# Performance work log

Hardware: AMD Instinct MI355X
Metric: run time of the kernel (lower is better)

## Reference

```python
import jax, jax.numpy as jnp
import numpy as np

N = 50000      # nodes
E = 625000     # edges
D_IN = 128     # in_feats
D_OUT = 128    # out_feats


def setup_inputs() -> dict:
    key = jax.random.key(0)
    k1, k2, k3, k4, k5, k6 = jax.random.split(key, 6)
    feat = jax.random.normal(k1, (N, D_IN), dtype=jnp.float32)
    affine = jax.random.uniform(k2, (E,), dtype=jnp.float32)
    src = jax.random.randint(k3, (E,), 0, N, dtype=jnp.int32)
    dst = jnp.sort(jax.random.randint(k4, (E,), 0, N, dtype=jnp.int32))
    # Linear(in_feats*2, out_feats): torch stores weight [out, in]; use [in, out] here
    bound = 1.0 / np.sqrt(2 * D_IN)
    W = jax.random.uniform(k5, (2 * D_IN, D_OUT), minval=-bound, maxval=bound, dtype=jnp.float32)
    b = jax.random.uniform(k6, (D_OUT,), minval=-bound, maxval=bound, dtype=jnp.float32)
    return {"feat": feat, "affine": affine, "src": src, "dst": dst, "W": W, "b": b}


def reference(feat, affine, src, dst, W, b):
    # u_mul_e: per-edge message = srcfeat[src] * edge scalar 'affine'
    msg = feat[src] * affine[:, None]                      # [E, D_IN]
    # fn.sum: scatter-add messages to destination nodes
    agg = jax.ops.segment_sum(msg, dst, num_segments=N)    # [N, D_IN]
    # concat dst features with aggregated neighborhood, then linear
    gcn_feat = jnp.concatenate([feat, agg], axis=-1)       # [N, 2*D_IN]
    return gcn_feat @ W + b                                # [N, D_OUT]
```

## Files before the change

### kernel.cpp

```cpp
#include <hip/hip_runtime.h>

#define N_NODES 50000
#define E_EDGES 625000
#define D 128

typedef __attribute__((ext_vector_type(8)))  short  short8;
typedef __attribute__((ext_vector_type(16))) float  floatx16;

static __device__ inline unsigned short f2bf(float f) {
    union { float f; unsigned u; } v; v.f = f;
    unsigned r = v.u + 0x7FFFu + ((v.u >> 16) & 1u);
    return (unsigned short)(r >> 16);
}
static __device__ inline float bflo(unsigned p) { return __uint_as_float(p << 16); }
static __device__ inline float bfhi(unsigned p) { return __uint_as_float(p & 0xFFFF0000u); }

__global__ __launch_bounds__(256) void prep_kernel(const int* __restrict__ dst,
                                                   const float* __restrict__ W,
                                                   int* __restrict__ rowptr,
                                                   unsigned short* __restrict__ wimg) {
    int t = blockIdx.x * 256 + threadIdx.x;
    if (t <= N_NODES) {
        int lo = 0, hi = E_EDGES;
        while (lo < hi) {
            int mid = (lo + hi) >> 1;
            if (dst[mid] < t) lo = mid + 1; else hi = mid;
        }
        rowptr[t] = lo;
    }
    if (t < 4096) {
        int n = t & 127;
        int c = (t >> 7) & 15;
        int h = t >> 11;
        int krow = h * 128 + c * 8;
        short8 v;
        #pragma unroll
        for (int j = 0; j < 8; ++j)
            v[j] = (short)f2bf(W[(size_t)(krow + j) * D + n]);
        *((short8*)wimg + t) = v;
    }
}

#define NB_M 391

__global__ __launch_bounds__(256, 3) void gemm_mfma(const float* __restrict__ feat,
                                                    const unsigned short* __restrict__ wimg,
                                                    const float* __restrict__ bias,
                                                    float* __restrict__ out,
                                                    unsigned short* __restrict__ Y) {
    __shared__ short8 Bls[2048];

    int tid = threadIdx.x;
    int idx = blockIdx.x;
    int h   = (idx >> 3) & 1;
    int b   = ((idx >> 4) << 3) | (idx & 7);
    if (b >= NB_M) return;

    const short8* wsrc = (const short8*)wimg + h * 2048;
    #pragma unroll
    for (int i = 0; i < 8; ++i)
        Bls[tid + i * 256] = wsrc[tid + i * 256];

    int wave = tid >> 6;
    int lane = tid & 63;
    int m = lane & 31;
    int g = lane >> 5;
    int row0   = b * 128 + wave * 32;
    int row_a  = row0 + m;
    int rclamp = row_a < N_NODES ? row_a : 0;

    short8 fa[8];
    const float* ap = feat + (size_t)rclamp * D + g * 8;
    #pragma unroll
    for (int ks = 0; ks < 8; ++ks) {
        float4 u = *(const float4*)(ap + ks * 16);
        float4 v = *(const float4*)(ap + ks * 16 + 4);
        short8 a;
        a[0] = (short)f2bf(u.x); a[1] = (short)f2bf(u.y);
        a[2] = (short)f2bf(u.z); a[3] = (short)f2bf(u.w);
        a[4] = (short)f2bf(v.x); a[5] = (short)f2bf(v.y);
        a[6] = (short)f2bf(v.z); a[7] = (short)f2bf(v.w);
        fa[ks] = a;
    }
    __syncthreads();

    #pragma unroll
    for (int t4 = 0; t4 < 4; ++t4) {
        int n = t4 * 32 + m;
        floatx16 acc = {0,0,0,0, 0,0,0,0, 0,0,0,0, 0,0,0,0};
        #pragma unroll
        for (int ks = 0; ks < 8; ++ks) {
            short8 bb = Bls[(ks * 2 + g) * 128 + n];
            acc = __builtin_amdgcn_mfma_f32_32x32x16_bf16(fa[ks], bb, acc, 0, 0, 0);
        }
        if (h == 0) {
            float bv = bias[n];
            #pragma unroll
            for (int r = 0; r < 16; ++r) {
                int row = row0 + (r & 3) + 8 * (r >> 2) + 4 * g;
                if (row < N_NODES) out[(size_t)row * D + n] = acc[r] + bv;
            }
        } else {
            #pragma unroll
            for (int r = 0; r < 16; ++r) {
                int row = row0 + (r & 3) + 8 * (r >> 2) + 4 * g;
                if (row < N_NODES) Y[(size_t)row * D + n] = f2bf(acc[r]);
            }
        }
    }
}

__global__ __launch_bounds__(256) void agg_add(const unsigned short* __restrict__ Y,
                                               const float* __restrict__ affine,
                                               const int* __restrict__ src,
                                               const int* __restrict__ rowptr,
                                               float* __restrict__ out) {
    int wave = threadIdx.x >> 6;
    int lane = threadIdx.x & 63;
    int n = blockIdx.x * 4 + wave;
    if (n >= N_NODES) return;
    int lo = rowptr[n], hi = rowptr[n + 1];
    int g  = lane >> 4;
    int jj = (lane & 15) << 3;

    float acc[8] = {0,0,0,0,0,0,0,0};
    const unsigned short* Yj = Y + jj;

    int e = lo;
    for (; e + 8 <= hi; e += 8) {
        int i0 = e + g,  i1 = e + 4 + g;
        int s0 = src[i0];  float w0 = affine[i0];
        int s1 = src[i1];  float w1 = affine[i1];
        uint4 p0 = *(const uint4*)(Yj + (size_t)s0 * D);
        uint4 p1 = *(const uint4*)(Yj + (size_t)s1 * D);
        acc[0] += bflo(p0.x) * w0;  acc[1] += bfhi(p0.x) * w0;
        acc[2] += bflo(p0.y) * w0;  acc[3] += bfhi(p0.y) * w0;
        acc[4] += bflo(p0.z) * w0;  acc[5] += bfhi(p0.z) * w0;
        acc[6] += bflo(p0.w) * w0;  acc[7] += bfhi(p0.w) * w0;
        acc[0] += bflo(p1.x) * w1;  acc[1] += bfhi(p1.x) * w1;
        acc[2] += bflo(p1.y) * w1;  acc[3] += bfhi(p1.y) * w1;
        acc[4] += bflo(p1.z) * w1;  acc[5] += bfhi(p1.z) * w1;
        acc[6] += bflo(p1.w) * w1;  acc[7] += bfhi(p1.w) * w1;
    }
    for (; e < hi; e += 4) {
        int  i = e + g;
        bool v = i < hi;
        int   s = src[v ? i : lo];
        float w = v ? affine[i] : 0.f;
        uint4 p = *(const uint4*)(Yj + (size_t)s * D);
        acc[0] += bflo(p.x) * w;  acc[1] += bfhi(p.x) * w;
        acc[2] += bflo(p.y) * w;  acc[3] += bfhi(p.y) * w;
        acc[4] += bflo(p.z) * w;  acc[5] += bfhi(p.z) * w;
        acc[6] += bflo(p.w) * w;  acc[7] += bfhi(p.w) * w;
    }

    #pragma unroll
    for (int r = 0; r < 8; ++r) {
        acc[r] += __shfl_xor(acc[r], 16);
        acc[r] += __shfl_xor(acc[r], 32);
    }

    if (g == 0) {
        float* op = out + (size_t)n * D + jj;
        float4 z0 = *(const float4*)op;
        float4 z1 = *(const float4*)(op + 4);
        z0.x += acc[0]; z0.y += acc[1]; z0.z += acc[2]; z0.w += acc[3];
        z1.x += acc[4]; z1.y += acc[5]; z1.z += acc[6]; z1.w += acc[7];
        *(float4*)op       = z0;
        *(float4*)(op + 4) = z1;
    }
}

extern "C" void kernel_launch(void* const* d_in, const int* in_sizes, int n_in,
                              void* d_out, int out_size, void* d_ws, size_t ws_size,
                              hipStream_t stream) {
    const float* feat   = (const float*)d_in[0];
    const float* affine = (const float*)d_in[1];
    const int*   src    = (const int*)  d_in[2];
    const int*   dst    = (const int*)  d_in[3];
    const float* W      = (const float*)d_in[4];
    const float* bias   = (const float*)d_in[5];
    float*       out    = (float*)d_out;

    unsigned short* wimg   = (unsigned short*)d_ws;
    int*            rowptr = (int*)((char*)d_ws + 65536);
    unsigned short* Y      = (unsigned short*)((char*)d_ws + 266240);

    prep_kernel<<<196, 256, 0, stream>>>(dst, W, rowptr, wimg);
    int gemm_blocks = ((2 * NB_M + 15) / 16) * 16;
    gemm_mfma<<<gemm_blocks, 256, 0, stream>>>(feat, wimg, bias, out, Y);
    agg_add<<<(N_NODES + 3) / 4, 256, 0, stream>>>(Y, affine, src, rowptr, out);
}
```

Before: 137.8 us.

## Interleave src/affine into packed edge metadata and unroll gather by four

The prep kernel now also packs each edge's src index and affine weight into one 8-byte record, launched over all edges. The aggregation kernel reads that record with a single load and processes 16 edges per iteration, four per lane group, issuing four independent row gathers before accumulating. The aim is fewer separate index/weight loads and more memory-level parallelism in the gather. In exchange it adds an extra 5 MB write plus read of edge metadata and a larger prep launch, and tail edges are masked rather than skipped.

```diff
diff --git a/kernel.cpp b/kernel.cpp
--- a/kernel.cpp
+++ b/kernel.cpp
@@ -17,8 +17,11 @@
 
 __global__ __launch_bounds__(256) void prep_kernel(const int* __restrict__ dst,
                                                    const float* __restrict__ W,
+                                                   const int* __restrict__ src,
+                                                   const float* __restrict__ affine,
                                                    int* __restrict__ rowptr,
-                                                   unsigned short* __restrict__ wimg) {
+                                                   unsigned short* __restrict__ wimg,
+                                                   uint2* __restrict__ meta) {
     int t = blockIdx.x * 256 + threadIdx.x;
     if (t <= N_NODES) {
         int lo = 0, hi = E_EDGES;
@@ -38,6 +41,12 @@
         for (int j = 0; j < 8; ++j)
             v[j] = (short)f2bf(W[(size_t)(krow + j) * D + n]);
         *((short8*)wimg + t) = v;
+    }
+    if (t < E_EDGES) {
+        uint2 m;
+        m.x = (unsigned)src[t];
+        m.y = __float_as_uint(affine[t]);
+        meta[t] = m;
     }
 }
 
@@ -111,8 +120,7 @@
 }
 
 __global__ __launch_bounds__(256) void agg_add(const unsigned short* __restrict__ Y,
-                                               const float* __restrict__ affine,
-                                               const int* __restrict__ src,
+                                               const uint2* __restrict__ meta,
                                                const int* __restrict__ rowptr,
                                                float* __restrict__ out) {
     int wave = threadIdx.x >> 6;
@@ -122,36 +130,32 @@
     int lo = rowptr[n], hi = rowptr[n + 1];
     int g  = lane >> 4;
     int jj = (lane & 15) << 3;
+    const unsigned short* Yj = Y + jj;
 
     float acc[8] = {0,0,0,0,0,0,0,0};
-    const unsigned short* Yj = Y + jj;
 
-    int e = lo;
-    for (; e + 8 <= hi; e += 8) {
-        int i0 = e + g,  i1 = e + 4 + g;
-        int s0 = src[i0];  float w0 = affine[i0];
-        int s1 = src[i1];  float w1 = affine[i1];
-        uint4 p0 = *(const uint4*)(Yj + (size_t)s0 * D);
-        uint4 p1 = *(const uint4*)(Yj + (size_t)s1 * D);
-        acc[0] += bflo(p0.x) * w0;  acc[1] += bfhi(p0.x) * w0;
-        acc[2] += bflo(p0.y) * w0;  acc[3] += bfhi(p0.y) * w0;
-        acc[4] += bflo(p0.z) * w0;  acc[5] += bfhi(p0.z) * w0;
-        acc[6] += bflo(p0.w) * w0;  acc[7] += bfhi(p0.w) * w0;
-        acc[0] += bflo(p1.x) * w1;  acc[1] += bfhi(p1.x) * w1;
-        acc[2] += bflo(p1.y) * w1;  acc[3] += bfhi(p1.y) * w1;
-        acc[4] += bflo(p1.z) * w1;  acc[5] += bfhi(p1.z) * w1;
-        acc[6] += bflo(p1.w) * w1;  acc[7] += bfhi(p1.w) * w1;
-    }
-    for (; e < hi; e += 4) {
-        int  i = e + g;
-        bool v = i < hi;
-        int   s = src[v ? i : lo];
-        float w = v ? affine[i] : 0.f;
-        uint4 p = *(const uint4*)(Yj + (size_t)s * D);
-        acc[0] += bflo(p.x) * w;  acc[1] += bfhi(p.x) * w;
-        acc[2] += bflo(p.y) * w;  acc[3] += bfhi(p.y) * w;
-        acc[4] += bflo(p.z) * w;  acc[5] += bfhi(p.z) * w;
-        acc[6] += bflo(p.w) * w;  acc[7] += bfhi(p.w) * w;
+    for (int e0 = lo; e0 < hi; e0 += 16) {
+        uint2 md[4];
+        #pragma unroll
+        for (int u = 0; u < 4; ++u) {
+            int i = e0 + u * 4 + g;
+            md[u] = meta[i < hi ? i : lo];
+        }
+        float w[4];
+        uint4 p[4];
+        #pragma unroll
+        for (int u = 0; u < 4; ++u) {
+            int i = e0 + u * 4 + g;
+            w[u] = (i < hi) ? __uint_as_float(md[u].y) : 0.f;
+            p[u] = *(const uint4*)(Yj + (size_t)md[u].x * D);
+        }
+        #pragma unroll
+        for (int u = 0; u < 4; ++u) {
+            acc[0] += bflo(p[u].x) * w[u];  acc[1] += bfhi(p[u].x) * w[u];
+            acc[2] += bflo(p[u].y) * w[u];  acc[3] += bfhi(p[u].y) * w[u];
+            acc[4] += bflo(p[u].z) * w[u];  acc[5] += bfhi(p[u].z) * w[u];
+            acc[6] += bflo(p[u].w) * w[u];  acc[7] += bfhi(p[u].w) * w[u];
+        }
     }
 
     #pragma unroll
@@ -184,10 +188,12 @@
 
     unsigned short* wimg   = (unsigned short*)d_ws;
     int*            rowptr = (int*)((char*)d_ws + 65536);
-    unsigned short* Y      = (unsigned short*)((char*)d_ws + 266240);
+    uint2*          meta   = (uint2*)((char*)d_ws + 266240);
+    unsigned short* Y      = (unsigned short*)((char*)d_ws + 5267456);
 
-    prep_kernel<<<196, 256, 0, stream>>>(dst, W, rowptr, wimg);
+    prep_kernel<<<(E_EDGES + 255) / 256, 256, 0, stream>>>(dst, W, src, affine,
+                                                           rowptr, wimg, meta);
     int gemm_blocks = ((2 * NB_M + 15) / 16) * 16;
     gemm_mfma<<<gemm_blocks, 256, 0, stream>>>(feat, wimg, bias, out, Y);
-    agg_add<<<(N_NODES + 3) / 4, 256, 0, stream>>>(Y, affine, src, rowptr, out);
+    agg_add<<<(N_NODES + 3) / 4, 256, 0, stream>>>(Y, meta, rowptr, out);
 }
```

New measurement: 135.4 us. Within noise of the previous version (-1.8%).
